# Kernel optimization log

Measured on AMD Instinct MI355X. Metric: run time of the kernel, lower is better.

The kernel has to match this reference:

```python
import jax, jax.numpy as jnp
import numpy as np

NEG = -10000.0


def _build_label_vocab():
    vocab = {'O': 0}
    i = 1
    for t in ['PER', 'ORG', 'LOC', 'MISC']:
        for p in ['B', 'I', 'E', 'S']:
            vocab[f'{p}-{t}'] = i
            i += 1
    return vocab


def _init_transition(key):
    """Random transition with BIOES constraints, matching CRF.initialize()."""
    vocab = _build_label_vocab()
    L = len(vocab) + 2          # 19 (17 labels + start + end)
    start, end = L - 2, L - 1
    T = np.array(jax.random.normal(key, (L, L)), dtype=np.float32)
    T[:, end] = NEG
    T[start, :] = NEG
    for lf, i_f in vocab.items():
        pf, tf = ('O', 'O') if lf == 'O' else lf.split('-')
        for lt, i_t in vocab.items():
            pt, tt = ('O', 'O') if lt == 'O' else lt.split('-')
            allowed = (pf in ('O', 'E', 'S') and pt in ('O', 'B', 'S')) or \
                      (pf in ('B', 'I') and pt in ('I', 'E') and tf == tt)
            if not allowed:
                T[i_t, i_f] = NEG
    return jnp.asarray(T)


def setup_inputs() -> dict:
    key = jax.random.key(0)
    k1, k2, k3, k4 = jax.random.split(key, 4)
    B, S, NL = 4096, 256, 17
    logits = jax.random.normal(k1, (B, S, NL), dtype=jnp.float32)
    labels = jax.random.randint(k2, (B, S), 0, NL)
    lens = jax.random.randint(k3, (B,), 1, S + 1)   # lengths in [1, S]
    transition = _init_transition(k4)                # [19, 19]
    return {"logits": logits, "labels": labels, "lens": lens,
            "transition": transition}


def reference(logits, labels, lens, transition):
    """CRF log-likelihood: gold_score(pad_logits(logits)) - norm_score."""
    B, S, NL = logits.shape
    L = transition.shape[0]       # label_size = NL + 2
    start, end = L - 2, L - 1

    # pad_logits: append start/end columns with -10000
    pads = jnp.full((B, S, 2), NEG, dtype=logits.dtype)
    logits_p = jnp.concatenate([logits, pads], axis=2)   # [B, S, L]

    tmask = (jnp.arange(S)[None, :] < lens[:, None])     # [B, S] valid tokens

    # ---- gold score ----
    # unary: gather emission score of the gold label at each position
    unary = jnp.take_along_axis(logits_p, labels[:, :, None], axis=2)[:, :, 0]
    unary = (unary * tmask.astype(logits.dtype)).sum(axis=1)

    # binary: transition scores along the gold path (with start/end padding)
    labels_ext = jnp.concatenate(
        [jnp.full((B, 1), start, labels.dtype), labels,
         jnp.full((B, 1), end, labels.dtype)], axis=1)   # [B, S+2]
    emask = jnp.arange(S + 2)[None, :] < (lens + 1)[:, None]
    labels_ext = jnp.where(emask, labels_ext, end)
    trn_scr = transition[labels_ext[:, 1:], labels_ext[:, :-1]]  # [B, S+1]
    bmask = (jnp.arange(S + 1)[None, :] < (lens + 1)[:, None]).astype(logits.dtype)
    binary = (trn_scr * bmask).sum(axis=1)

    gold = unary + binary

    # ---- partition (norm) score: forward algorithm over time ----
    alpha0 = jnp.full((B, L), NEG, dtype=logits.dtype).at[:, start].set(0.0)

    def step(alpha, xs):
        logit, m = xs  # logit: [B, L], m: [B] bool (position < len)
        # alpha_nxt[b,i] = logit[b,i] + LSE_j(alpha[b,j] + T[i,j])
        nxt = logit + jax.nn.logsumexp(alpha[:, None, :] + transition[None], axis=2)
        alpha = jnp.where(m[:, None], nxt, alpha)
        return alpha, None

    alpha, _ = jax.lax.scan(step, alpha0,
                            (jnp.swapaxes(logits_p, 0, 1), tmask.T))
    alpha = alpha + transition[end][None, :]
    norm = jax.nn.logsumexp(alpha, axis=1)

    return gold - norm   # [B] per-sequence log-likelihood
```

## Files before the change

kernel.cpp:

```cpp
#include <hip/hip_runtime.h>

constexpr int S    = 256;
constexpr int NL   = 17;
constexpr int L    = 19;
constexpr int CAPB = 16384;

typedef float v4 __attribute__((ext_vector_type(4), aligned(4)));

__device__ float g_Z[CAPB * 17];
__device__ float g_V[CAPB * 17];
__device__ float g_mf[CAPB];
__device__ float g_mv[CAPB];

#define ROWF(X,i) X(i,0) X(i,3) X(i,4) X(i,7) X(i,8) X(i,11) X(i,12) X(i,15) X(i,16)
#define FWD_ALL(X) \
  ROWF(X,0) ROWF(X,1) ROWF(X,4) ROWF(X,5) ROWF(X,8) ROWF(X,9) ROWF(X,12) ROWF(X,13) ROWF(X,16) \
  X(2,1) X(2,2) X(3,1) X(3,2) X(6,5) X(6,6) X(7,5) X(7,6) \
  X(10,9) X(10,10) X(11,9) X(11,10) X(14,13) X(14,14) X(15,13) X(15,14)

#define ROWB(X,i) X(i,0) X(i,1) X(i,4) X(i,5) X(i,8) X(i,9) X(i,12) X(i,13) X(i,16)
#define BWD_ALL(X) \
  ROWB(X,0) ROWB(X,3) ROWB(X,4) ROWB(X,7) ROWB(X,8) ROWB(X,11) ROWB(X,12) ROWB(X,15) ROWB(X,16) \
  X(1,2) X(1,3) X(2,2) X(2,3) X(5,6) X(5,7) X(6,6) X(6,7) \
  X(9,10) X(9,11) X(10,10) X(10,11) X(13,14) X(13,15) X(14,14) X(14,15)

#define APPLY17(X) X(0) X(1) X(2) X(3) X(4) X(5) X(6) X(7) X(8) X(9) X(10) X(11) X(12) X(13) X(14) X(15) X(16)

#define DCF_F(i,j) const float cf_##i##_##j = __expf(Tg[(i)*19+(j)]);
#define DCF_B(i,j) const float cf_##i##_##j = __expf(Tg[(j)*19+(i)]);

#define DPF(i) float p##i = __expf(Tg[(i)*19+17]);
#define DPB(i) float p##i = __expf(Tg[18*19+(i)]);

#define DECLSLOT(T) float T##0,T##1,T##2,T##3,T##4,T##5,T##6,T##7,T##8,T##9, \
                          T##10,T##11,T##12,T##13,T##14,T##15,T##16;

#define LOADTOK(T, OFF) { \
    const char* a_ = base + (OFF); \
    const v4 x0_ = *(const v4*)(a_); \
    const v4 x1_ = *(const v4*)(a_ + 16); \
    const v4 x2_ = *(const v4*)(a_ + 32); \
    const v4 x3_ = *(const v4*)(a_ + 48); \
    const float x4_ = *(const float*)(a_ + 64); \
    T##0=x0_.x; T##1=x0_.y; T##2=x0_.z; T##3=x0_.w; \
    T##4=x1_.x; T##5=x1_.y; T##6=x1_.z; T##7=x1_.w; \
    T##8=x2_.x; T##9=x2_.y; T##10=x2_.z; T##11=x2_.w; \
    T##12=x3_.x; T##13=x3_.y; T##14=x3_.z; T##15=x3_.w; T##16=x4_; }

#define MKQALL(T) \
    const float q0 = __expf(T##0) * p0;   const float q1 = __expf(T##1) * p1; \
    const float q2 = __expf(T##2) * p2;   const float q3 = __expf(T##3) * p3; \
    const float q4 = __expf(T##4) * p4;   const float q5 = __expf(T##5) * p5; \
    const float q6 = __expf(T##6) * p6;   const float q7 = __expf(T##7) * p7; \
    const float q8 = __expf(T##8) * p8;   const float q9 = __expf(T##9) * p9; \
    const float q10 = __expf(T##10) * p10; const float q11 = __expf(T##11) * p11; \
    const float q12 = __expf(T##12) * p12; const float q13 = __expf(T##13) * p13; \
    const float q14 = __expf(T##14) * p14; const float q15 = __expf(T##15) * p15; \
    const float q16 = __expf(T##16) * p16;

#define FMQ(i,j) cf_##i##_##j * q##j
#define ROW9N(i,a,b,c,d,e,f,g,h,k) \
    const float n##i = (((FMQ(i,a)+FMQ(i,b)) + (FMQ(i,c)+FMQ(i,d))) + \
                        ((FMQ(i,e)+FMQ(i,f)) + (FMQ(i,g)+FMQ(i,h)))) + FMQ(i,k);
#define ROW2N(i,a,b) const float n##i = FMQ(i,a) + FMQ(i,b);

#define MATVEC_F \
    ROW9N(0,0,3,4,7,8,11,12,15,16)  ROW9N(1,0,3,4,7,8,11,12,15,16) \
    ROW9N(4,0,3,4,7,8,11,12,15,16)  ROW9N(5,0,3,4,7,8,11,12,15,16) \
    ROW9N(8,0,3,4,7,8,11,12,15,16)  ROW9N(9,0,3,4,7,8,11,12,15,16) \
    ROW9N(12,0,3,4,7,8,11,12,15,16) ROW9N(13,0,3,4,7,8,11,12,15,16) \
    ROW9N(16,0,3,4,7,8,11,12,15,16) \
    ROW2N(2,1,2)   ROW2N(3,1,2)   ROW2N(6,5,6)   ROW2N(7,5,6) \
    ROW2N(10,9,10) ROW2N(11,9,10) ROW2N(14,13,14) ROW2N(15,13,14)

#define MATVEC_B \
    ROW9N(0,0,1,4,5,8,9,12,13,16)  ROW9N(3,0,1,4,5,8,9,12,13,16) \
    ROW9N(4,0,1,4,5,8,9,12,13,16)  ROW9N(7,0,1,4,5,8,9,12,13,16) \
    ROW9N(8,0,1,4,5,8,9,12,13,16)  ROW9N(11,0,1,4,5,8,9,12,13,16) \
    ROW9N(12,0,1,4,5,8,9,12,13,16) ROW9N(15,0,1,4,5,8,9,12,13,16) \
    ROW9N(16,0,1,4,5,8,9,12,13,16) \
    ROW2N(1,2,3)   ROW2N(2,2,3)   ROW2N(5,6,7)   ROW2N(6,6,7) \
    ROW2N(9,10,11) ROW2N(10,10,11) ROW2N(13,14,15) ROW2N(14,14,15)

#define ASG(i)  p##i = n##i;
#define ASGR(i) p##i = n##i * r_;

#define STORE_P { \
    float* d_ = SC + bc * 17; \
    d_[0]=p0; d_[1]=p1; d_[2]=p2; d_[3]=p3; d_[4]=p4; d_[5]=p5; d_[6]=p6; d_[7]=p7; \
    d_[8]=p8; d_[9]=p9; d_[10]=p10; d_[11]=p11; d_[12]=p12; d_[13]=p13; d_[14]=p14; \
    d_[15]=p15; d_[16]=p16; \
    SM[bc] = m; }

#define CHAINSTEP(T, T_, OFFV, RN, MV, DOCLAMP, SSTR) { \
    MKQALL(T) \
    OFFV += (SSTR); \
    if (DOCLAMP) { if (OFFV < capLo) OFFV = capLo; } \
    LOADTOK(T, OFFV) \
    MV \
    if (RN) { \
        float mxA = fmaxf(fmaxf(n0,n1),  fmaxf(n2,n3)); \
        float mxB = fmaxf(fmaxf(n4,n5),  fmaxf(n6,n7)); \
        float mxC = fmaxf(fmaxf(n8,n9),  fmaxf(n10,n11)); \
        float mxD = fmaxf(fmaxf(n12,n13),fmaxf(n14,n15)); \
        float mx  = fmaxf(fmaxf(fmaxf(mxA,mxB), fmaxf(mxC,mxD)), n16); \
        const float r_ = __frcp_rn(mx); \
        m += __logf(mx); \
        APPLY17(ASGR) \
    } else { \
        APPLY17(ASG) \
    } \
    if ((T_) == nup - 1) STORE_P \
}

__device__ __forceinline__ void chainF(const float* __restrict__ logits,
                                       const int* __restrict__ lens,
                                       const float* __restrict__ Tg, int B, int z)
{
    const int  lane  = threadIdx.x;
    const int  braw  = z * 64 + lane;
    const bool valid = braw < B;
    const int  bc    = valid ? braw : 0;
    const int  len   = lens[bc];
    const int  mid   = len >> 1;
    const int  nup   = valid ? mid : 0;

    FWD_ALL(DCF_F)
    APPLY17(DPF)
    float  m  = 0.0f;
    float* SC = g_Z;
    float* SM = g_mf;
    if (nup == 0 && valid) STORE_P

    int nmax = nup;
    #pragma unroll
    for (int o = 32; o >= 1; o >>= 1) nmax = max(nmax, __shfl_xor(nmax, o));
    nmax = (nmax + 3) & ~3;

    const char* base  = (const char*)logits;
    const int   sb4   = bc * (S * NL * 4);
    const int   capLo = sb4;
    int off0 = sb4, off1 = sb4 + 68, off2 = sb4 + 136, off3 = sb4 + 204;

    DECLSLOT(sA) DECLSLOT(sB) DECLSLOT(sC) DECLSLOT(sD)
    LOADTOK(sA, off0) LOADTOK(sB, off1) LOADTOK(sC, off2) LOADTOK(sD, off3)

    for (int tb = 0; tb < nmax; tb += 4) {
        CHAINSTEP(sA, tb,     off0, 0, MATVEC_F, 0, 272)
        CHAINSTEP(sB, tb + 1, off1, 0, MATVEC_F, 0, 272)
        CHAINSTEP(sC, tb + 2, off2, 0, MATVEC_F, 0, 272)
        CHAINSTEP(sD, tb + 3, off3, 1, MATVEC_F, 0, 272)
    }
}

__device__ __forceinline__ void chainB(const float* __restrict__ logits,
                                       const int* __restrict__ lens,
                                       const float* __restrict__ Tg, int B, int z)
{
    const int  lane  = threadIdx.x;
    const int  braw  = z * 64 + lane;
    const bool valid = braw < B;
    const int  bc    = valid ? braw : 0;
    const int  len   = lens[bc];
    const int  mid   = len >> 1;
    const int  nup   = valid ? (len - 1 - mid) : 0;

    BWD_ALL(DCF_B)
    APPLY17(DPB)
    float  m  = 0.0f;
    float* SC = g_V;
    float* SM = g_mv;
    if (nup == 0 && valid) STORE_P

    int nmax = nup;
    #pragma unroll
    for (int o = 32; o >= 1; o >>= 1) nmax = max(nmax, __shfl_xor(nmax, o));
    nmax = (nmax + 3) & ~3;

    const char* base  = (const char*)logits;
    const int   sb4   = bc * (S * NL * 4);
    const int   capLo = sb4;
    const int   t0    = len - 1;
    int off0 = sb4 + max(t0,     0) * 68;
    int off1 = sb4 + max(t0 - 1, 0) * 68;
    int off2 = sb4 + max(t0 - 2, 0) * 68;
    int off3 = sb4 + max(t0 - 3, 0) * 68;

    DECLSLOT(sA) DECLSLOT(sB) DECLSLOT(sC) DECLSLOT(sD)
    LOADTOK(sA, off0) LOADTOK(sB, off1) LOADTOK(sC, off2) LOADTOK(sD, off3)

    for (int tb = 0; tb < nmax; tb += 4) {
        CHAINSTEP(sA, tb,     off0, 0, MATVEC_B, 1, -272)
        CHAINSTEP(sB, tb + 1, off1, 0, MATVEC_B, 1, -272)
        CHAINSTEP(sC, tb + 2, off2, 0, MATVEC_B, 1, -272)
        CHAINSTEP(sD, tb + 3, off3, 1, MATVEC_B, 1, -272)
    }
}

__global__ __launch_bounds__(64, 1)
void crf_chain(const float* __restrict__ logits, const int* __restrict__ lens,
               const float* __restrict__ Tg, int B, int nbh)
{
    if ((int)blockIdx.x < nbh) chainF(logits, lens, Tg, B, blockIdx.x);
    else                       chainB(logits, lens, Tg, B, blockIdx.x - nbh);
}

__global__ __launch_bounds__(64)
void crf_combine(const float* __restrict__ logits, const int* __restrict__ labels,
                 const int* __restrict__ lens, const float* __restrict__ T,
                 float* __restrict__ out, int B)
{
    const int b    = blockIdx.x;
    const int wtid = threadIdx.x;
    const int len  = lens[b];
    const int mid  = len >> 1;

    float prod = 0.0f;
    if (wtid < 17) {
        const float z  = g_Z[b * 17 + wtid];
        const float v  = g_V[b * 17 + wtid];
        const float lg = logits[(size_t)b * (S * NL) + mid * NL + wtid];
        prod = z * v * __expf(lg);
    }
    #pragma unroll
    for (int o = 32; o >= 1; o >>= 1) prod += __shfl_xor(prod, o);
    const float norm = g_mf[b] + g_mv[b] + __logf(prod);

    const int* labp = labels + b * S;
    float gsum = 0.0f;
    for (int c = 0; c < len; c += 64) {
        const int tok = c + wtid;
        if (tok < len) {
            const int lab = labp[tok];
            const int prv = (tok == 0) ? (L - 2) : labp[tok - 1];
            gsum += logits[(size_t)b * (S * NL) + tok * NL + lab] + T[lab * L + prv];
        }
    }
    #pragma unroll
    for (int o = 32; o >= 1; o >>= 1) gsum += __shfl_xor(gsum, o);
    const float gold = gsum + T[(L - 1) * L + labp[len - 1]];

    if (wtid == 0) out[b] = gold - norm;
}

extern "C" void kernel_launch(void* const* d_in, const int* in_sizes, int n_in,
                              void* d_out, int out_size, void* d_ws, size_t ws_size,
                              hipStream_t stream)
{
    (void)n_in; (void)out_size; (void)d_ws; (void)ws_size;
    const float* logits     = (const float*)d_in[0];
    const int*   labels     = (const int*)d_in[1];
    const int*   lens       = (const int*)d_in[2];
    const float* transition = (const float*)d_in[3];
    float*       out        = (float*)d_out;
    const int B   = in_sizes[2];
    const int NBH = (B + 63) / 64;

    crf_chain<<<dim3(2 * NBH), dim3(64), 0, stream>>>(logits, lens, transition, B, NBH);
    crf_combine<<<dim3(B), dim3(64), 0, stream>>>(logits, labels, lens, transition, out, B);
}
```

Before: 168.0 us.

## Stage logits chunks into LDS via global_load_lds with coalesced wave loads

```diff
diff --git a/kernel.cpp b/kernel.cpp
--- a/kernel.cpp
+++ b/kernel.cpp
@@ -4,13 +4,17 @@
 constexpr int NL   = 17;
 constexpr int L    = 19;
 constexpr int CAPB = 16384;
-
-typedef float v4 __attribute__((ext_vector_type(4), aligned(4)));
+constexpr int CT   = 12;
+constexpr int LSTR = CT * NL + 1;
 
 __device__ float g_Z[CAPB * 17];
 __device__ float g_V[CAPB * 17];
 __device__ float g_mf[CAPB];
 __device__ float g_mv[CAPB];
+
+typedef const __attribute__((address_space(1))) unsigned int gu32;
+typedef __attribute__((address_space(3))) unsigned int lu32;
+#define GLL(GP, LP) __builtin_amdgcn_global_load_lds((GP), (LP), 4, 0, 0)
 
 #define ROWF(X,i) X(i,0) X(i,3) X(i,4) X(i,7) X(i,8) X(i,11) X(i,12) X(i,15) X(i,16)
 #define FWD_ALL(X) \
@@ -35,17 +39,11 @@
 #define DECLSLOT(T) float T##0,T##1,T##2,T##3,T##4,T##5,T##6,T##7,T##8,T##9, \
                           T##10,T##11,T##12,T##13,T##14,T##15,T##16;
 
-#define LOADTOK(T, OFF) { \
-    const char* a_ = base + (OFF); \
-    const v4 x0_ = *(const v4*)(a_); \
-    const v4 x1_ = *(const v4*)(a_ + 16); \
-    const v4 x2_ = *(const v4*)(a_ + 32); \
-    const v4 x3_ = *(const v4*)(a_ + 48); \
-    const float x4_ = *(const float*)(a_ + 64); \
-    T##0=x0_.x; T##1=x0_.y; T##2=x0_.z; T##3=x0_.w; \
-    T##4=x1_.x; T##5=x1_.y; T##6=x1_.z; T##7=x1_.w; \
-    T##8=x2_.x; T##9=x2_.y; T##10=x2_.z; T##11=x2_.w; \
-    T##12=x3_.x; T##13=x3_.y; T##14=x3_.z; T##15=x3_.w; T##16=x4_; }
+#define LOADSLOT(T, LAB) { \
+    const float* la_ = (const float*)(ldsB + (LAB)); \
+    T##0=la_[0]; T##1=la_[1]; T##2=la_[2]; T##3=la_[3]; T##4=la_[4]; T##5=la_[5]; \
+    T##6=la_[6]; T##7=la_[7]; T##8=la_[8]; T##9=la_[9]; T##10=la_[10]; T##11=la_[11]; \
+    T##12=la_[12]; T##13=la_[13]; T##14=la_[14]; T##15=la_[15]; T##16=la_[16]; }
 
 #define MKQALL(T) \
     const float q0 = __expf(T##0) * p0;   const float q1 = __expf(T##1) * p1; \
@@ -92,11 +90,9 @@
     d_[15]=p15; d_[16]=p16; \
     SM[bc] = m; }
 
-#define CHAINSTEP(T, T_, OFFV, RN, MV, DOCLAMP, SSTR) { \
-    MKQALL(T) \
-    OFFV += (SSTR); \
-    if (DOCLAMP) { if (OFFV < capLo) OFFV = capLo; } \
-    LOADTOK(T, OFFV) \
+#define CSTEP(CUR, NXT, T_, LAB, RN, MV) { \
+    MKQALL(CUR) \
+    LOADSLOT(NXT, LAB) \
     MV \
     if (RN) { \
         float mxA = fmaxf(fmaxf(n0,n1),  fmaxf(n2,n3)); \
@@ -115,7 +111,8 @@
 
 __device__ __forceinline__ void chainF(const float* __restrict__ logits,
                                        const int* __restrict__ lens,
-                                       const float* __restrict__ Tg, int B, int z)
+                                       const float* __restrict__ Tg,
+                                       int B, int z, float* ldsbuf)
 {
     const int  lane  = threadIdx.x;
     const int  braw  = z * 64 + lane;
@@ -135,27 +132,40 @@
     int nmax = nup;
     #pragma unroll
     for (int o = 32; o >= 1; o >>= 1) nmax = max(nmax, __shfl_xor(nmax, o));
-    nmax = (nmax + 3) & ~3;
-
-    const char* base  = (const char*)logits;
-    const int   sb4   = bc * (S * NL * 4);
-    const int   capLo = sb4;
-    int off0 = sb4, off1 = sb4 + 68, off2 = sb4 + 136, off3 = sb4 + 204;
-
-    DECLSLOT(sA) DECLSLOT(sB) DECLSLOT(sC) DECLSLOT(sD)
-    LOADTOK(sA, off0) LOADTOK(sB, off1) LOADTOK(sC, off2) LOADTOK(sD, off3)
-
-    for (int tb = 0; tb < nmax; tb += 4) {
-        CHAINSTEP(sA, tb,     off0, 0, MATVEC_F, 0, 272)
-        CHAINSTEP(sB, tb + 1, off1, 0, MATVEC_F, 0, 272)
-        CHAINSTEP(sC, tb + 2, off2, 0, MATVEC_F, 0, 272)
-        CHAINSTEP(sD, tb + 3, off3, 1, MATVEC_F, 0, 272)
+    const int nch = (nmax + CT - 1) / CT;
+
+    const char* ldsB = (const char*)ldsbuf + lane * (LSTR * 4);
+    gu32* gall = (gu32*)(const void*)logits;
+    lu32* lall = (lu32*)(void*)ldsbuf;
+    DECLSLOT(cv) DECLSLOT(nv)
+
+    for (int c = 0; c < nch; ++c) {
+        const int tbase = c * CT;
+        for (int j = 0; j < 64; ++j) {
+            const int bj  = z * 64 + j;
+            const int bjc = bj < B ? bj : 0;
+            gu32* gp = gall + (unsigned)bjc * (S * NL) + (unsigned)tbase * NL + lane;
+            lu32* lp = lall + j * LSTR;
+            GLL(gp,       lp);
+            GLL(gp + 64,  lp + 64);
+            GLL(gp + 128, lp + 128);
+            if (lane < CT * NL - 192) GLL(gp + 192, lp + 192);
+        }
+        asm volatile("s_waitcnt vmcnt(0)" ::: "memory");
+        LOADSLOT(cv, 0)
+        #pragma unroll
+        for (int u = 0; u < CT; u += 2) {
+            CSTEP(cv, nv, tbase + u,     (u + 1) * 68, false, MATVEC_F)
+            CSTEP(nv, cv, tbase + u + 1, (u + 2 < CT ? u + 2 : CT - 1) * 68,
+                  ((u & 2) != 0), MATVEC_F)
+        }
     }
 }
 
 __device__ __forceinline__ void chainB(const float* __restrict__ logits,
                                        const int* __restrict__ lens,
-                                       const float* __restrict__ Tg, int B, int z)
+                                       const float* __restrict__ Tg,
+                                       int B, int z, float* ldsbuf)
 {
     const int  lane  = threadIdx.x;
     const int  braw  = z * 64 + lane;
@@ -175,25 +185,39 @@
     int nmax = nup;
     #pragma unroll
     for (int o = 32; o >= 1; o >>= 1) nmax = max(nmax, __shfl_xor(nmax, o));
-    nmax = (nmax + 3) & ~3;
-
-    const char* base  = (const char*)logits;
-    const int   sb4   = bc * (S * NL * 4);
-    const int   capLo = sb4;
-    const int   t0    = len - 1;
-    int off0 = sb4 + max(t0,     0) * 68;
-    int off1 = sb4 + max(t0 - 1, 0) * 68;
-    int off2 = sb4 + max(t0 - 2, 0) * 68;
-    int off3 = sb4 + max(t0 - 3, 0) * 68;
-
-    DECLSLOT(sA) DECLSLOT(sB) DECLSLOT(sC) DECLSLOT(sD)
-    LOADTOK(sA, off0) LOADTOK(sB, off1) LOADTOK(sC, off2) LOADTOK(sD, off3)
-
-    for (int tb = 0; tb < nmax; tb += 4) {
-        CHAINSTEP(sA, tb,     off0, 0, MATVEC_B, 1, -272)
-        CHAINSTEP(sB, tb + 1, off1, 0, MATVEC_B, 1, -272)
-        CHAINSTEP(sC, tb + 2, off2, 0, MATVEC_B, 1, -272)
-        CHAINSTEP(sD, tb + 3, off3, 1, MATVEC_B, 1, -272)
+    const int nch = (nmax + CT - 1) / CT;
+
+    const char* ldsB = (const char*)ldsbuf + lane * (LSTR * 4);
+    gu32* gall = (gu32*)(const void*)logits;
+    lu32* lall = (lu32*)(void*)ldsbuf;
+    DECLSLOT(cv) DECLSLOT(nv)
+
+    for (int c = 0; c < nch; ++c) {
+        const int tbase = c * CT;
+        for (int j = 0; j < 64; ++j) {
+            const int bj   = z * 64 + j;
+            const int bjc  = bj < B ? bj : 0;
+            const int lenj = __shfl(len, j);
+            const int btok = max(lenj - CT - tbase, 0);
+            gu32* gp = gall + (unsigned)bjc * (S * NL) + (unsigned)btok * NL + lane;
+            lu32* lp = lall + j * LSTR;
+            GLL(gp,       lp);
+            GLL(gp + 64,  lp + 64);
+            GLL(gp + 128, lp + 128);
+            if (lane < CT * NL - 192) GLL(gp + 192, lp + 192);
+        }
+        asm volatile("s_waitcnt vmcnt(0)" ::: "memory");
+        const int bt = max(len - CT - tbase, 0);
+        int dof = min(max(len - 1 - tbase - bt, 0), CT - 1);
+        LOADSLOT(cv, dof * 68)
+        #pragma unroll
+        for (int u = 0; u < CT; u += 2) {
+            const int dn1 = max(dof - 1, 0);
+            CSTEP(cv, nv, tbase + u,     dn1 * 68, false, MATVEC_B)
+            const int dn2 = max(dn1 - 1, 0);
+            CSTEP(nv, cv, tbase + u + 1, dn2 * 68, ((u & 2) != 0), MATVEC_B)
+            dof = dn2;
+        }
     }
 }
 
@@ -201,8 +225,9 @@
 void crf_chain(const float* __restrict__ logits, const int* __restrict__ lens,
                const float* __restrict__ Tg, int B, int nbh)
 {
-    if ((int)blockIdx.x < nbh) chainF(logits, lens, Tg, B, blockIdx.x);
-    else                       chainB(logits, lens, Tg, B, blockIdx.x - nbh);
+    __shared__ float ldsbuf[64 * LSTR];
+    if ((int)blockIdx.x < nbh) chainF(logits, lens, Tg, B, blockIdx.x, ldsbuf);
+    else                       chainB(logits, lens, Tg, B, blockIdx.x - nbh, ldsbuf);
 }
 
 __global__ __launch_bounds__(64)
```

After: 233.8 us. 39.2% more time.

## Pack CRF chain matvec into paired float2 FMAs and shorten prefetch depth

Applied to the files above, without the earlier changes.

```diff
diff --git a/kernel.cpp b/kernel.cpp
--- a/kernel.cpp
+++ b/kernel.cpp
@@ -6,111 +6,206 @@
 constexpr int CAPB = 16384;
 
 typedef float v4 __attribute__((ext_vector_type(4), aligned(4)));
+typedef float f2 __attribute__((ext_vector_type(2)));
 
 __device__ float g_Z[CAPB * 17];
 __device__ float g_V[CAPB * 17];
 __device__ float g_mf[CAPB];
 __device__ float g_mv[CAPB];
 
-#define ROWF(X,i) X(i,0) X(i,3) X(i,4) X(i,7) X(i,8) X(i,11) X(i,12) X(i,15) X(i,16)
-#define FWD_ALL(X) \
-  ROWF(X,0) ROWF(X,1) ROWF(X,4) ROWF(X,5) ROWF(X,8) ROWF(X,9) ROWF(X,12) ROWF(X,13) ROWF(X,16) \
-  X(2,1) X(2,2) X(3,1) X(3,2) X(6,5) X(6,6) X(7,5) X(7,6) \
-  X(10,9) X(10,10) X(11,9) X(11,10) X(14,13) X(14,14) X(15,13) X(15,14)
-
-#define ROWB(X,i) X(i,0) X(i,1) X(i,4) X(i,5) X(i,8) X(i,9) X(i,12) X(i,13) X(i,16)
-#define BWD_ALL(X) \
-  ROWB(X,0) ROWB(X,3) ROWB(X,4) ROWB(X,7) ROWB(X,8) ROWB(X,11) ROWB(X,12) ROWB(X,15) ROWB(X,16) \
-  X(1,2) X(1,3) X(2,2) X(2,3) X(5,6) X(5,7) X(6,6) X(6,7) \
-  X(9,10) X(9,11) X(10,10) X(10,11) X(13,14) X(13,15) X(14,14) X(14,15)
-
-#define APPLY17(X) X(0) X(1) X(2) X(3) X(4) X(5) X(6) X(7) X(8) X(9) X(10) X(11) X(12) X(13) X(14) X(15) X(16)
-
-#define DCF_F(i,j) const float cf_##i##_##j = __expf(Tg[(i)*19+(j)]);
-#define DCF_B(i,j) const float cf_##i##_##j = __expf(Tg[(j)*19+(i)]);
-
-#define DPF(i) float p##i = __expf(Tg[(i)*19+17]);
-#define DPB(i) float p##i = __expf(Tg[18*19+(i)]);
-
-#define DECLSLOT(T) float T##0,T##1,T##2,T##3,T##4,T##5,T##6,T##7,T##8,T##9, \
-                          T##10,T##11,T##12,T##13,T##14,T##15,T##16;
-
-#define LOADTOK(T, OFF) { \
+__device__ __forceinline__ f2 mkf2(float a, float b) { f2 r; r.x = a; r.y = b; return r; }
+__device__ __forceinline__ f2 dup2(float a)          { f2 r; r.x = a; r.y = a; return r; }
+#define FMA2(A,B,C) __builtin_elementwise_fma((A),(B),(C))
+#define MAX2(A,B)   __builtin_elementwise_max((A),(B))
+
+
+#define CWF(K,a,b,j) const f2 c##K##_##j = mkf2(__expf(Tg[(a)*19+(j)]), __expf(Tg[(b)*19+(j)]));
+#define CWB(K,a,b,j) const f2 c##K##_##j = mkf2(__expf(Tg[(j)*19+(a)]), __expf(Tg[(j)*19+(b)]));
+#define WCOLS_F(X,K,a,b) X(K,a,b,0) X(K,a,b,3) X(K,a,b,4) X(K,a,b,7) X(K,a,b,8) X(K,a,b,11) X(K,a,b,12) X(K,a,b,15) X(K,a,b,16)
+#define WCOLS_B(X,K,a,b) X(K,a,b,0) X(K,a,b,1) X(K,a,b,4) X(K,a,b,5) X(K,a,b,8) X(K,a,b,9) X(K,a,b,12) X(K,a,b,13) X(K,a,b,16)
+
+#define COEF_F \
+  WCOLS_F(CWF,0,0,1) WCOLS_F(CWF,1,4,5) WCOLS_F(CWF,2,8,9) WCOLS_F(CWF,3,12,13) \
+  CWF(4,2,3,1) CWF(4,2,3,2) CWF(5,6,7,5) CWF(5,6,7,6) \
+  CWF(6,10,11,9) CWF(6,10,11,10) CWF(7,14,15,13) CWF(7,14,15,14) \
+  const float c16_0 = __expf(Tg[16*19+0]);  const float c16_3 = __expf(Tg[16*19+3]); \
+  const float c16_4 = __expf(Tg[16*19+4]);  const float c16_7 = __expf(Tg[16*19+7]); \
+  const float c16_8 = __expf(Tg[16*19+8]);  const float c16_11 = __expf(Tg[16*19+11]); \
+  const float c16_12 = __expf(Tg[16*19+12]); const float c16_15 = __expf(Tg[16*19+15]); \
+  const float c16_16 = __expf(Tg[16*19+16]);
+
+#define COEF_B \
+  WCOLS_B(CWB,0,0,3) WCOLS_B(CWB,1,4,7) WCOLS_B(CWB,2,8,11) WCOLS_B(CWB,3,12,15) \
+  CWB(4,1,2,2) CWB(4,1,2,3) CWB(5,5,6,6) CWB(5,5,6,7) \
+  CWB(6,9,10,10) CWB(6,9,10,11) CWB(7,13,14,14) CWB(7,13,14,15) \
+  const float c16_0 = __expf(Tg[0*19+16]);  const float c16_1 = __expf(Tg[1*19+16]); \
+  const float c16_4 = __expf(Tg[4*19+16]);  const float c16_5 = __expf(Tg[5*19+16]); \
+  const float c16_8 = __expf(Tg[8*19+16]);  const float c16_9 = __expf(Tg[9*19+16]); \
+  const float c16_12 = __expf(Tg[12*19+16]); const float c16_13 = __expf(Tg[13*19+16]); \
+  const float c16_16f = __expf(Tg[16*19+16]);
+
+#define PINIT_F \
+  f2 vP0 = mkf2(__expf(Tg[0*19+17]),  __expf(Tg[1*19+17])); \
+  f2 vP1 = mkf2(__expf(Tg[4*19+17]),  __expf(Tg[5*19+17])); \
+  f2 vP2 = mkf2(__expf(Tg[8*19+17]),  __expf(Tg[9*19+17])); \
+  f2 vP3 = mkf2(__expf(Tg[12*19+17]), __expf(Tg[13*19+17])); \
+  f2 vP4 = mkf2(__expf(Tg[2*19+17]),  __expf(Tg[3*19+17])); \
+  f2 vP5 = mkf2(__expf(Tg[6*19+17]),  __expf(Tg[7*19+17])); \
+  f2 vP6 = mkf2(__expf(Tg[10*19+17]), __expf(Tg[11*19+17])); \
+  f2 vP7 = mkf2(__expf(Tg[14*19+17]), __expf(Tg[15*19+17])); \
+  float vp16 = __expf(Tg[16*19+17]);
+
+#define PINIT_B \
+  f2 vP0 = mkf2(__expf(Tg[18*19+0]),  __expf(Tg[18*19+3])); \
+  f2 vP1 = mkf2(__expf(Tg[18*19+4]),  __expf(Tg[18*19+7])); \
+  f2 vP2 = mkf2(__expf(Tg[18*19+8]),  __expf(Tg[18*19+11])); \
+  f2 vP3 = mkf2(__expf(Tg[18*19+12]), __expf(Tg[18*19+15])); \
+  f2 vP4 = mkf2(__expf(Tg[18*19+1]),  __expf(Tg[18*19+2])); \
+  f2 vP5 = mkf2(__expf(Tg[18*19+5]),  __expf(Tg[18*19+6])); \
+  f2 vP6 = mkf2(__expf(Tg[18*19+9]),  __expf(Tg[18*19+10])); \
+  f2 vP7 = mkf2(__expf(Tg[18*19+13]), __expf(Tg[18*19+14])); \
+  float vp16 = __expf(Tg[18*19+16]);
+
+#define DECLSLOT2(T) f2 T##0,T##1,T##2,T##3,T##4,T##5,T##6,T##7; float T##16;
+
+#define LOADF(SL, OFF) { \
     const char* a_ = base + (OFF); \
-    const v4 x0_ = *(const v4*)(a_); \
-    const v4 x1_ = *(const v4*)(a_ + 16); \
-    const v4 x2_ = *(const v4*)(a_ + 32); \
-    const v4 x3_ = *(const v4*)(a_ + 48); \
-    const float x4_ = *(const float*)(a_ + 64); \
-    T##0=x0_.x; T##1=x0_.y; T##2=x0_.z; T##3=x0_.w; \
-    T##4=x1_.x; T##5=x1_.y; T##6=x1_.z; T##7=x1_.w; \
-    T##8=x2_.x; T##9=x2_.y; T##10=x2_.z; T##11=x2_.w; \
-    T##12=x3_.x; T##13=x3_.y; T##14=x3_.z; T##15=x3_.w; T##16=x4_; }
-
-#define MKQALL(T) \
-    const float q0 = __expf(T##0) * p0;   const float q1 = __expf(T##1) * p1; \
-    const float q2 = __expf(T##2) * p2;   const float q3 = __expf(T##3) * p3; \
-    const float q4 = __expf(T##4) * p4;   const float q5 = __expf(T##5) * p5; \
-    const float q6 = __expf(T##6) * p6;   const float q7 = __expf(T##7) * p7; \
-    const float q8 = __expf(T##8) * p8;   const float q9 = __expf(T##9) * p9; \
-    const float q10 = __expf(T##10) * p10; const float q11 = __expf(T##11) * p11; \
-    const float q12 = __expf(T##12) * p12; const float q13 = __expf(T##13) * p13; \
-    const float q14 = __expf(T##14) * p14; const float q15 = __expf(T##15) * p15; \
-    const float q16 = __expf(T##16) * p16;
-
-#define FMQ(i,j) cf_##i##_##j * q##j
-#define ROW9N(i,a,b,c,d,e,f,g,h,k) \
-    const float n##i = (((FMQ(i,a)+FMQ(i,b)) + (FMQ(i,c)+FMQ(i,d))) + \
-                        ((FMQ(i,e)+FMQ(i,f)) + (FMQ(i,g)+FMQ(i,h)))) + FMQ(i,k);
-#define ROW2N(i,a,b) const float n##i = FMQ(i,a) + FMQ(i,b);
-
-#define MATVEC_F \
-    ROW9N(0,0,3,4,7,8,11,12,15,16)  ROW9N(1,0,3,4,7,8,11,12,15,16) \
-    ROW9N(4,0,3,4,7,8,11,12,15,16)  ROW9N(5,0,3,4,7,8,11,12,15,16) \
-    ROW9N(8,0,3,4,7,8,11,12,15,16)  ROW9N(9,0,3,4,7,8,11,12,15,16) \
-    ROW9N(12,0,3,4,7,8,11,12,15,16) ROW9N(13,0,3,4,7,8,11,12,15,16) \
-    ROW9N(16,0,3,4,7,8,11,12,15,16) \
-    ROW2N(2,1,2)   ROW2N(3,1,2)   ROW2N(6,5,6)   ROW2N(7,5,6) \
-    ROW2N(10,9,10) ROW2N(11,9,10) ROW2N(14,13,14) ROW2N(15,13,14)
-
-#define MATVEC_B \
-    ROW9N(0,0,1,4,5,8,9,12,13,16)  ROW9N(3,0,1,4,5,8,9,12,13,16) \
-    ROW9N(4,0,1,4,5,8,9,12,13,16)  ROW9N(7,0,1,4,5,8,9,12,13,16) \
-    ROW9N(8,0,1,4,5,8,9,12,13,16)  ROW9N(11,0,1,4,5,8,9,12,13,16) \
-    ROW9N(12,0,1,4,5,8,9,12,13,16) ROW9N(15,0,1,4,5,8,9,12,13,16) \
-    ROW9N(16,0,1,4,5,8,9,12,13,16) \
-    ROW2N(1,2,3)   ROW2N(2,2,3)   ROW2N(5,6,7)   ROW2N(6,6,7) \
-    ROW2N(9,10,11) ROW2N(10,10,11) ROW2N(13,14,15) ROW2N(14,14,15)
-
-#define ASG(i)  p##i = n##i;
-#define ASGR(i) p##i = n##i * r_;
-
-#define STORE_P { \
-    float* d_ = SC + bc * 17; \
-    d_[0]=p0; d_[1]=p1; d_[2]=p2; d_[3]=p3; d_[4]=p4; d_[5]=p5; d_[6]=p6; d_[7]=p7; \
-    d_[8]=p8; d_[9]=p9; d_[10]=p10; d_[11]=p11; d_[12]=p12; d_[13]=p13; d_[14]=p14; \
-    d_[15]=p15; d_[16]=p16; \
-    SM[bc] = m; }
-
-#define CHAINSTEP(T, T_, OFFV, RN, MV, DOCLAMP, SSTR) { \
-    MKQALL(T) \
-    OFFV += (SSTR); \
-    if (DOCLAMP) { if (OFFV < capLo) OFFV = capLo; } \
-    LOADTOK(T, OFFV) \
-    MV \
+    const v4 x0 = *(const v4*)(a_);      const v4 x1 = *(const v4*)(a_ + 16); \
+    const v4 x2 = *(const v4*)(a_ + 32); const v4 x3 = *(const v4*)(a_ + 48); \
+    const float x4 = *(const float*)(a_ + 64); \
+    SL##0 = mkf2(x0.x, x0.y); SL##4 = mkf2(x0.z, x0.w); \
+    SL##1 = mkf2(x1.x, x1.y); SL##5 = mkf2(x1.z, x1.w); \
+    SL##2 = mkf2(x2.x, x2.y); SL##6 = mkf2(x2.z, x2.w); \
+    SL##3 = mkf2(x3.x, x3.y); SL##7 = mkf2(x3.z, x3.w); \
+    SL##16 = x4; }
+
+#define LOADB(SL, OFF) { \
+    const char* a_ = base + (OFF); \
+    const v4 x0 = *(const v4*)(a_);      const v4 x1 = *(const v4*)(a_ + 16); \
+    const v4 x2 = *(const v4*)(a_ + 32); const v4 x3 = *(const v4*)(a_ + 48); \
+    const float x4 = *(const float*)(a_ + 64); \
+    SL##0 = mkf2(x0.x, x0.w); SL##4 = mkf2(x0.y, x0.z); \
+    SL##1 = mkf2(x1.x, x1.w); SL##5 = mkf2(x1.y, x1.z); \
+    SL##2 = mkf2(x2.x, x2.w); SL##6 = mkf2(x2.y, x2.z); \
+    SL##3 = mkf2(x3.x, x3.w); SL##7 = mkf2(x3.y, x3.z); \
+    SL##16 = x4; }
+
+#define MKQ(SL) \
+    const f2 Q0 = mkf2(__expf((SL##0).x), __expf((SL##0).y)) * vP0; \
+    const f2 Q1 = mkf2(__expf((SL##1).x), __expf((SL##1).y)) * vP1; \
+    const f2 Q2 = mkf2(__expf((SL##2).x), __expf((SL##2).y)) * vP2; \
+    const f2 Q3 = mkf2(__expf((SL##3).x), __expf((SL##3).y)) * vP3; \
+    const f2 Q4 = mkf2(__expf((SL##4).x), __expf((SL##4).y)) * vP4; \
+    const f2 Q5 = mkf2(__expf((SL##5).x), __expf((SL##5).y)) * vP5; \
+    const f2 Q6 = mkf2(__expf((SL##6).x), __expf((SL##6).y)) * vP6; \
+    const f2 Q7 = mkf2(__expf((SL##7).x), __expf((SL##7).y)) * vP7; \
+    const float q16 = __expf(SL##16) * vp16;
+
+#define DUPS_F \
+    const f2 d0=dup2(Q0.x), d3=dup2(Q4.y), d4=dup2(Q1.x), d7=dup2(Q5.y), \
+             d8=dup2(Q2.x), d11=dup2(Q6.y), d12=dup2(Q3.x), d15=dup2(Q7.y), d16=dup2(q16); \
+    const f2 d1=dup2(Q0.y), d2=dup2(Q4.x), d5=dup2(Q1.y), d6=dup2(Q5.x), \
+             d9=dup2(Q2.y), d10=dup2(Q6.x), d13=dup2(Q3.y), d14=dup2(Q7.x);
+
+#define DUPS_B \
+    const f2 d0=dup2(Q0.x), d1=dup2(Q4.x), d4=dup2(Q1.x), d5=dup2(Q5.x), \
+             d8=dup2(Q2.x), d9=dup2(Q6.x), d12=dup2(Q3.x), d13=dup2(Q7.x), d16=dup2(q16); \
+    const f2 d2=dup2(Q4.y), d3=dup2(Q0.y), d6=dup2(Q5.y), d7=dup2(Q1.y), \
+             d10=dup2(Q6.y), d11=dup2(Q2.y), d14=dup2(Q7.y), d15=dup2(Q3.y);
+
+#define WROW_F(K) \
+    f2 N##K = c##K##_0 * d0; \
+    N##K = FMA2(c##K##_3,  d3,  N##K); N##K = FMA2(c##K##_4,  d4,  N##K); \
+    N##K = FMA2(c##K##_7,  d7,  N##K); N##K = FMA2(c##K##_8,  d8,  N##K); \
+    N##K = FMA2(c##K##_11, d11, N##K); N##K = FMA2(c##K##_12, d12, N##K); \
+    N##K = FMA2(c##K##_15, d15, N##K); N##K = FMA2(c##K##_16, d16, N##K);
+
+#define WROW_B(K) \
+    f2 N##K = c##K##_0 * d0; \
+    N##K = FMA2(c##K##_1,  d1,  N##K); N##K = FMA2(c##K##_4,  d4,  N##K); \
+    N##K = FMA2(c##K##_5,  d5,  N##K); N##K = FMA2(c##K##_8,  d8,  N##K); \
+    N##K = FMA2(c##K##_9,  d9,  N##K); N##K = FMA2(c##K##_12, d12, N##K); \
+    N##K = FMA2(c##K##_13, d13, N##K); N##K = FMA2(c##K##_16, d16, N##K);
+
+#define NARROW_F \
+    f2 N4 = c4_1 * d1;   N4 = FMA2(c4_2,  d2,  N4); \
+    f2 N5 = c5_5 * d5;   N5 = FMA2(c5_6,  d6,  N5); \
+    f2 N6 = c6_9 * d9;   N6 = FMA2(c6_10, d10, N6); \
+    f2 N7 = c7_13 * d13; N7 = FMA2(c7_14, d14, N7);
+
+#define NARROW_B \
+    f2 N4 = c4_2 * d2;   N4 = FMA2(c4_3,  d3,  N4); \
+    f2 N5 = c5_6 * d6;   N5 = FMA2(c5_7,  d7,  N5); \
+    f2 N6 = c6_10 * d10; N6 = FMA2(c6_11, d11, N6); \
+    f2 N7 = c7_14 * d14; N7 = FMA2(c7_15, d15, N7);
+
+#define R16_F \
+    float n16 = c16_0 * d0.x; \
+    n16 = fmaf(c16_3, d3.x, n16);   n16 = fmaf(c16_4, d4.x, n16); \
+    n16 = fmaf(c16_7, d7.x, n16);   n16 = fmaf(c16_8, d8.x, n16); \
+    n16 = fmaf(c16_11, d11.x, n16); n16 = fmaf(c16_12, d12.x, n16); \
+    n16 = fmaf(c16_15, d15.x, n16); n16 = fmaf(c16_16, d16.x, n16);
+
+#define R16_B \
+    float n16 = c16_0 * d0.x; \
+    n16 = fmaf(c16_1, d1.x, n16);   n16 = fmaf(c16_4, d4.x, n16); \
+    n16 = fmaf(c16_5, d5.x, n16);   n16 = fmaf(c16_8, d8.x, n16); \
+    n16 = fmaf(c16_9, d9.x, n16);   n16 = fmaf(c16_12, d12.x, n16); \
+    n16 = fmaf(c16_13, d13.x, n16); n16 = fmaf(c16_16f, d16.x, n16);
+
+#define FINISH(RN) \
     if (RN) { \
-        float mxA = fmaxf(fmaxf(n0,n1),  fmaxf(n2,n3)); \
-        float mxB = fmaxf(fmaxf(n4,n5),  fmaxf(n6,n7)); \
-        float mxC = fmaxf(fmaxf(n8,n9),  fmaxf(n10,n11)); \
-        float mxD = fmaxf(fmaxf(n12,n13),fmaxf(n14,n15)); \
-        float mx  = fmaxf(fmaxf(fmaxf(mxA,mxB), fmaxf(mxC,mxD)), n16); \
+        const f2 MM = MAX2(MAX2(MAX2(N0,N1), MAX2(N2,N3)), \
+                           MAX2(MAX2(N4,N5), MAX2(N6,N7))); \
+        const float mx = fmaxf(fmaxf(MM.x, MM.y), n16); \
         const float r_ = __frcp_rn(mx); \
         m += __logf(mx); \
-        APPLY17(ASGR) \
+        const f2 R2 = dup2(r_); \
+        vP0=N0*R2; vP1=N1*R2; vP2=N2*R2; vP3=N3*R2; \
+        vP4=N4*R2; vP5=N5*R2; vP6=N6*R2; vP7=N7*R2; vp16=n16*r_; \
     } else { \
-        APPLY17(ASG) \
-    } \
-    if ((T_) == nup - 1) STORE_P \
+        vP0=N0; vP1=N1; vP2=N2; vP3=N3; vP4=N4; vP5=N5; vP6=N6; vP7=N7; vp16=n16; \
+    }
+
+#define STOREF { \
+    float* d_ = g_Z + bc * 17; \
+    d_[0]=vP0.x;  d_[1]=vP0.y;  d_[2]=vP4.x;  d_[3]=vP4.y; \
+    d_[4]=vP1.x;  d_[5]=vP1.y;  d_[6]=vP5.x;  d_[7]=vP5.y; \
+    d_[8]=vP2.x;  d_[9]=vP2.y;  d_[10]=vP6.x; d_[11]=vP6.y; \
+    d_[12]=vP3.x; d_[13]=vP3.y; d_[14]=vP7.x; d_[15]=vP7.y; \
+    d_[16]=vp16;  g_mf[bc]=m; }
+
+#define STOREB { \
+    float* d_ = g_V + bc * 17; \
+    d_[0]=vP0.x;  d_[3]=vP0.y;  d_[1]=vP4.x;  d_[2]=vP4.y; \
+    d_[4]=vP1.x;  d_[7]=vP1.y;  d_[5]=vP5.x;  d_[6]=vP5.y; \
+    d_[8]=vP2.x;  d_[11]=vP2.y; d_[9]=vP6.x;  d_[10]=vP6.y; \
+    d_[12]=vP3.x; d_[15]=vP3.y; d_[13]=vP7.x; d_[14]=vP7.y; \
+    d_[16]=vp16;  g_mv[bc]=m; }
+
+#define CSTEPF(SL, T_, OFFV, RN) { \
+    MKQ(SL) \
+    OFFV += 136; \
+    LOADF(SL, OFFV) \
+    DUPS_F \
+    WROW_F(0) WROW_F(1) WROW_F(2) WROW_F(3) \
+    NARROW_F \
+    R16_F \
+    FINISH(RN) \
+    if ((T_) == nup - 1) STOREF \
+}
+
+#define CSTEPB(SL, T_, OFFV, RN) { \
+    MKQ(SL) \
+    OFFV -= 136; \
+    if (OFFV < capLo) OFFV = capLo; \
+    LOADB(SL, OFFV) \
+    DUPS_B \
+    WROW_B(0) WROW_B(1) WROW_B(2) WROW_B(3) \
+    NARROW_B \
+    R16_B \
+    FINISH(RN) \
+    if ((T_) == nup - 1) STOREB \
 }
 
 __device__ __forceinline__ void chainF(const float* __restrict__ logits,
@@ -125,31 +220,28 @@
     const int  mid   = len >> 1;
     const int  nup   = valid ? mid : 0;
 
-    FWD_ALL(DCF_F)
-    APPLY17(DPF)
-    float  m  = 0.0f;
-    float* SC = g_Z;
-    float* SM = g_mf;
-    if (nup == 0 && valid) STORE_P
+    COEF_F
+    PINIT_F
+    float m = 0.0f;
+    if (nup == 0 && valid) STOREF
 
     int nmax = nup;
     #pragma unroll
     for (int o = 32; o >= 1; o >>= 1) nmax = max(nmax, __shfl_xor(nmax, o));
     nmax = (nmax + 3) & ~3;
 
-    const char* base  = (const char*)logits;
-    const int   sb4   = bc * (S * NL * 4);
-    const int   capLo = sb4;
-    int off0 = sb4, off1 = sb4 + 68, off2 = sb4 + 136, off3 = sb4 + 204;
-
-    DECLSLOT(sA) DECLSLOT(sB) DECLSLOT(sC) DECLSLOT(sD)
-    LOADTOK(sA, off0) LOADTOK(sB, off1) LOADTOK(sC, off2) LOADTOK(sD, off3)
+    const char* base = (const char*)logits;
+    const int   sb4  = bc * (S * NL * 4);
+    int offA = sb4, offB = sb4 + 68;
+
+    DECLSLOT2(sA) DECLSLOT2(sB)
+    LOADF(sA, offA) LOADF(sB, offB)
 
     for (int tb = 0; tb < nmax; tb += 4) {
-        CHAINSTEP(sA, tb,     off0, 0, MATVEC_F, 0, 272)
-        CHAINSTEP(sB, tb + 1, off1, 0, MATVEC_F, 0, 272)
-        CHAINSTEP(sC, tb + 2, off2, 0, MATVEC_F, 0, 272)
-        CHAINSTEP(sD, tb + 3, off3, 1, MATVEC_F, 0, 272)
+        CSTEPF(sA, tb,     offA, 0)
+        CSTEPF(sB, tb + 1, offB, 0)
+        CSTEPF(sA, tb + 2, offA, 0)
+        CSTEPF(sB, tb + 3, offB, 1)
     }
 }
 
@@ -165,12 +257,10 @@
     const int  mid   = len >> 1;
     const int  nup   = valid ? (len - 1 - mid) : 0;
 
-    BWD_ALL(DCF_B)
-    APPLY17(DPB)
-    float  m  = 0.0f;
-    float* SC = g_V;
-    float* SM = g_mv;
-    if (nup == 0 && valid) STORE_P
+    COEF_B
+    PINIT_B
+    float m = 0.0f;
+    if (nup == 0 && valid) STOREB
 
     int nmax = nup;
     #pragma unroll
@@ -180,20 +270,17 @@
     const char* base  = (const char*)logits;
     const int   sb4   = bc * (S * NL * 4);
     const int   capLo = sb4;
-    const int   t0    = len - 1;
-    int off0 = sb4 + max(t0,     0) * 68;
-    int off1 = sb4 + max(t0 - 1, 0) * 68;
-    int off2 = sb4 + max(t0 - 2, 0) * 68;
-    int off3 = sb4 + max(t0 - 3, 0) * 68;
-
-    DECLSLOT(sA) DECLSLOT(sB) DECLSLOT(sC) DECLSLOT(sD)
-    LOADTOK(sA, off0) LOADTOK(sB, off1) LOADTOK(sC, off2) LOADTOK(sD, off3)
+    int offA = sb4 + max(len - 1, 0) * 68;
+    int offB = sb4 + max(len - 2, 0) * 68;
+
+    DECLSLOT2(sA) DECLSLOT2(sB)
+    LOADB(sA, offA) LOADB(sB, offB)
 
     for (int tb = 0; tb < nmax; tb += 4) {
-        CHAINSTEP(sA, tb,     off0, 0, MATVEC_B, 1, -272)
-        CHAINSTEP(sB, tb + 1, off1, 0, MATVEC_B, 1, -272)
-        CHAINSTEP(sC, tb + 2, off2, 0, MATVEC_B, 1, -272)
-        CHAINSTEP(sD, tb + 3, off3, 1, MATVEC_B, 1, -272)
+        CSTEPB(sA, tb,     offA, 0)
+        CSTEPB(sB, tb + 1, offB, 0)
+        CSTEPB(sA, tb + 2, offA, 0)
+        CSTEPB(sB, tb + 3, offB, 1)
     }
 }
 
```

After: 162.4 us. -3.3%, faster.
